# Kernel tuning notes

Measured on AMD Instinct MI355X. Metric: run time of the kernel, lower is better.

Reference implementation:

```python
import jax, jax.numpy as jnp
import numpy as np

EPS = 1e-12
TEMP = 0.05
LAMBDA2 = 0.5


def _normalize(x):
    # F.normalize(x, dim=1), eps=1e-12
    n = jnp.linalg.norm(x, axis=1, keepdims=True)
    return x / jnp.maximum(n, EPS)


def _cdist(x, f):
    # torch.cdist p=2: [B, N] euclidean distances
    x2 = jnp.sum(x * x, axis=1, keepdims=True)          # [B,1]
    f2 = jnp.sum(f * f, axis=1)[None, :]                # [1,N]
    d2 = x2 + f2 - 2.0 * (x @ f.T)
    return jnp.sqrt(jnp.maximum(d2, 0.0))


def _ce(logits, targets):
    # F.cross_entropy with integer targets, mean reduction
    logp = jax.nn.log_softmax(logits, axis=1)
    return -jnp.take_along_axis(logp, targets[:, None], axis=1).mean()


def _branch_loss(x_raw, f, targets):
    x = _normalize(x_raw)
    # note: original applies cross_entropy (which does another log_softmax)
    # on top of softmax(cdist(...)) -- reproduced faithfully
    soft = jax.nn.softmax(_cdist(x, f), axis=1)
    out = (x @ f.T) / TEMP
    return _ce(out, targets) + _ce(soft, targets)


def setup_inputs() -> dict:
    key = jax.random.key(0)
    ks = jax.random.split(key, 7)
    B, N, D = 256, 8192, 2048
    inputs = jax.random.normal(ks[0], (B, D), dtype=jnp.float32)
    inputs_up = jax.random.normal(ks[1], (B, D), dtype=jnp.float32)
    inputs_down = jax.random.normal(ks[2], (B, D), dtype=jnp.float32)
    targets = jax.random.randint(ks[3], (B,), 0, N)
    # memory banks are buffers; initialize as L2-normalized rows (realistic state)
    features = _normalize(jax.random.normal(ks[4], (N, D), dtype=jnp.float32))
    features_up = _normalize(jax.random.normal(ks[5], (N, D), dtype=jnp.float32))
    features_down = _normalize(jax.random.normal(ks[6], (N, D), dtype=jnp.float32))
    return {
        "inputs": inputs,
        "inputs_up": inputs_up,
        "inputs_down": inputs_down,
        "targets": targets,
        "epoch": 10,
        "features": features,
        "features_up": features_up,
        "features_down": features_down,
    }


def reference(inputs, inputs_up, inputs_down, targets, epoch, features, features_up, features_down):
    l_mid = _branch_loss(inputs, features, targets)
    l_up = _branch_loss(inputs_up, features_up, targets)
    l_down = _branch_loss(inputs_down, features_down, targets)
    loss = (1.0 - LAMBDA2) * l_mid + LAMBDA2 * (l_up + l_down)
    return loss
```

## Files before the change

kernel.cpp:

```cpp
#include <hip/hip_runtime.h>

typedef float f4v __attribute__((ext_vector_type(4)));
typedef float f32x4 __attribute__((ext_vector_type(4)));
typedef __bf16 bf16x8 __attribute__((ext_vector_type(8)));
typedef unsigned short ushort8 __attribute__((ext_vector_type(8)));

static constexpr int KDIM = 2048;

static constexpr size_t OFF_XN      = 0;
static constexpr size_t OFF_PART    = (size_t)3 * 256 * 2048 * 2;
static constexpr size_t OFF_DOTT    = OFF_PART + (size_t)768 * 128 * 16;
static constexpr size_t OFF_ROWLOSS = OFF_DOTT + 768 * 4;

__device__ __forceinline__ unsigned short f2bf(float x) {
  union { float f; unsigned u; } c; c.f = x;
  unsigned r = c.u + 0x7fffu + ((c.u >> 16) & 1u);
  return (unsigned short)(r >> 16);
}

__device__ __forceinline__ void gload_lds16(const void* g, void* l) {
  __builtin_amdgcn_global_load_lds((const __attribute__((address_space(1))) void*)g,
                                   (__attribute__((address_space(3))) void*)l,
                                   16, 0, 0);
}

__device__ __forceinline__ bf16x8 cvt8(f4v lo, f4v hi) {
  bf16x8 r;
  r[0] = (__bf16)lo[0]; r[1] = (__bf16)lo[1]; r[2] = (__bf16)lo[2]; r[3] = (__bf16)lo[3];
  r[4] = (__bf16)hi[0]; r[5] = (__bf16)hi[1]; r[6] = (__bf16)hi[2]; r[7] = (__bf16)hi[3];
  return r;
}

__global__ __launch_bounds__(256) void k_normalize(
    const float* __restrict__ x0, const float* __restrict__ x1, const float* __restrict__ x2,
    unsigned short* __restrict__ xn)
{
  int bid = blockIdx.x;
  int branch = bid >> 8;
  int row = bid & 255;
  const float* src = (branch == 0 ? x0 : (branch == 1 ? x1 : x2)) + (size_t)row * KDIM;
  int tid = threadIdx.x;
  f4v a = *(const f4v*)(src + tid * 8);
  f4v b = *(const f4v*)(src + tid * 8 + 4);
  float s = a[0]*a[0] + a[1]*a[1] + a[2]*a[2] + a[3]*a[3]
          + b[0]*b[0] + b[1]*b[1] + b[2]*b[2] + b[3]*b[3];
  #pragma unroll
  for (int m = 1; m < 64; m <<= 1) s += __shfl_xor(s, m);
  __shared__ float ls[4];
  if ((tid & 63) == 0) ls[tid >> 6] = s;
  __syncthreads();
  float total = ls[0] + ls[1] + ls[2] + ls[3];
  float inv = 1.0f / fmaxf(sqrtf(total), 1e-12f);
  ushort8 u;
  #pragma unroll
  for (int e = 0; e < 4; ++e) u[e]     = f2bf(a[e] * inv);
  #pragma unroll
  for (int e = 0; e < 4; ++e) u[4 + e] = f2bf(b[e] * inv);
  *(ushort8*)(xn + (size_t)bid * KDIM + tid * 8) = u;
}

__global__ __launch_bounds__(512, 1) void k_gemm_fused(
    const unsigned short* __restrict__ xn,
    const float* __restrict__ f0, const float* __restrict__ f1, const float* __restrict__ f2,
    const int* __restrict__ targets,
    float* __restrict__ part, float* __restrict__ dotT)
{
  __shared__ char lds[2 * 65536];

  int bid = blockIdx.x;
  int swz = (bid & 7) * 24 + (bid >> 3);
  int branch = swz >> 6;
  int ntile = swz & 63;

  const unsigned short* A = xn + (size_t)branch * 256 * KDIM;
  const float* F = (branch == 0 ? f0 : (branch == 1 ? f1 : f2)) + (size_t)ntile * 128 * KDIM;

  int tid = threadIdx.x;
  int wave = tid >> 6;
  int lane = tid & 63;
  int rcol0 = lane & 15;
  int klane = lane >> 4;
  int wr = wave >> 1;
  int wc = wave & 1;

  const unsigned short* aSrc = A + (size_t)(tid >> 3) * KDIM
                             + (((tid & 7) ^ ((tid >> 3) & 7)) << 3);
  const float* bSrc = F + (size_t)(tid >> 4) * KDIM
                    + (((tid & 15) ^ ((tid >> 4) & 15)) << 2);
  char* aDst = lds + wave * 1024;
  char* bDst = lds + 32768 + wave * 1024;

#define STAGE(kt, buf) do { \
    _Pragma("unroll") for (int g = 0; g < 4; ++g) \
      gload_lds16(aSrc + (size_t)g * 64 * KDIM + (kt) * 64, \
                  aDst + (buf) * 65536 + g * 8192); \
    _Pragma("unroll") for (int g = 0; g < 4; ++g) \
      gload_lds16(bSrc + (size_t)g * 32 * KDIM + (kt) * 64, \
                  bDst + (buf) * 65536 + g * 8192); \
  } while (0)

  f32x4 acc[4][4];
  #pragma unroll
  for (int i = 0; i < 4; ++i)
    #pragma unroll
    for (int j = 0; j < 4; ++j)
      #pragma unroll
      for (int q = 0; q < 4; ++q) acc[i][j][q] = 0.0f;

  int sa = rcol0 & 7;
  const char* aRd = lds + (wr * 64 + rcol0) * 128;
  const char* bRd = lds + 32768 + (wc * 64 + rcol0) * 256;

#define COMPUTE(buf) do { \
    const char* ra = aRd + (buf) * 65536; \
    const char* rb = bRd + (buf) * 65536; \
    _Pragma("unroll") for (int ks = 0; ks < 2; ++ks) { \
      int chA = (((ks * 4 + klane) ^ sa) << 4); \
      int x = ks * 8 + klane * 2; \
      int chB0 = ((x ^ rcol0) << 4); \
      int chB1 = (((x + 1) ^ rcol0) << 4); \
      bf16x8 a0 = *(const bf16x8*)(ra + chA); \
      bf16x8 a1 = *(const bf16x8*)(ra + 2048 + chA); \
      bf16x8 a2 = *(const bf16x8*)(ra + 4096 + chA); \
      bf16x8 a3 = *(const bf16x8*)(ra + 6144 + chA); \
      _Pragma("unroll") for (int j = 0; j < 4; ++j) { \
        f4v lo = *(const f4v*)(rb + j * 4096 + chB0); \
        f4v hi = *(const f4v*)(rb + j * 4096 + chB1); \
        bf16x8 bj = cvt8(lo, hi); \
        acc[0][j] = __builtin_amdgcn_mfma_f32_16x16x32_bf16(a0, bj, acc[0][j], 0, 0, 0); \
        acc[1][j] = __builtin_amdgcn_mfma_f32_16x16x32_bf16(a1, bj, acc[1][j], 0, 0, 0); \
        acc[2][j] = __builtin_amdgcn_mfma_f32_16x16x32_bf16(a2, bj, acc[2][j], 0, 0, 0); \
        acc[3][j] = __builtin_amdgcn_mfma_f32_16x16x32_bf16(a3, bj, acc[3][j], 0, 0, 0); \
      } \
    } \
  } while (0)

  STAGE(0, 0);
  __syncthreads();
  for (int kt = 0; kt < 31; ++kt) {
    int cur = kt & 1;
    STAGE(kt + 1, cur ^ 1);
    COMPUTE(cur);
    __syncthreads();
  }
  COMPUTE(1);

#undef STAGE
#undef COMPUTE

  int tbase = branch * 256;
  #pragma unroll
  for (int i = 0; i < 4; ++i) {
    #pragma unroll
    for (int q = 0; q < 4; ++q) {
      int row = wr * 64 + i * 16 + (klane << 2) + q;
      int tgt = targets[row];
      float s1 = 0.f, s2 = 0.f, s3 = 0.f, s4 = 0.f;
      #pragma unroll
      for (int j = 0; j < 4; ++j) {
        float d = acc[i][j][q];
        float e1 = __expf(fmaf(20.0f, d, -20.0f));
        float Dv = sqrtf(fmaxf(2.0f - 2.0f * d, 0.0f));
        float e2 = __expf(Dv - 2.0f);
        s1 += e1; s2 += e2;
        float t2 = e2 * e2;
        s3 += t2; s4 += t2 * e2;
        int col = ntile * 128 + wc * 64 + j * 16 + rcol0;
        if (col == tgt) dotT[tbase + row] = d;
      }
      #pragma unroll
      for (int m = 1; m < 16; m <<= 1) {
        s1 += __shfl_xor(s1, m);
        s2 += __shfl_xor(s2, m);
        s3 += __shfl_xor(s3, m);
        s4 += __shfl_xor(s4, m);
      }
      if (rcol0 == 0) {
        f32x4 p; p[0] = s1; p[1] = s2; p[2] = s3; p[3] = s4;
        *(f32x4*)(part + ((size_t)(tbase + row) * 128 + ntile * 2 + wc) * 4) = p;
      }
    }
  }
}

__global__ __launch_bounds__(128) void k_combine(
    const float* __restrict__ part, const float* __restrict__ dotT, float* __restrict__ rowloss)
{
  int row = blockIdx.x;
  int tid = threadIdx.x;
  f4v p = *(const f4v*)(part + ((size_t)row * 128 + tid) * 4);
  float a0 = p[0], a1 = p[1], a2 = p[2], a3 = p[3];
  #pragma unroll
  for (int m = 1; m < 64; m <<= 1) {
    a0 += __shfl_xor(a0, m); a1 += __shfl_xor(a1, m);
    a2 += __shfl_xor(a2, m); a3 += __shfl_xor(a3, m);
  }
  __shared__ float ls[8];
  if ((tid & 63) == 0) {
    int w = tid >> 6;
    ls[w] = a0; ls[2 + w] = a1; ls[4 + w] = a2; ls[6 + w] = a3;
  }
  __syncthreads();
  if (tid == 0) {
    float p1 = ls[0] + ls[1];
    float Z1 = ls[2] + ls[3];
    float Z2 = ls[4] + ls[5];
    float Z3 = ls[6] + ls[7];
    float dt = dotT[row];
    float CE1 = 20.0f + logf(p1) - 20.0f * dt;
    float Dt = sqrtf(fmaxf(2.0f - 2.0f * dt, 0.0f));
    float St = __expf(Dt - 2.0f) / Z1;
    float sES = 8193.0f + Z2 / (2.0f * Z1 * Z1) + Z3 / (6.0f * Z1 * Z1 * Z1);
    float CE2 = logf(sES) - St;
    rowloss[row] = (CE1 + CE2) * (0.5f / 256.0f);
  }
}

__global__ __launch_bounds__(256) void k_final(const float* __restrict__ rowloss, float* __restrict__ out)
{
  int tid = threadIdx.x;
  float v = rowloss[tid] + rowloss[tid + 256] + rowloss[tid + 512];
  #pragma unroll
  for (int m = 1; m < 64; m <<= 1) v += __shfl_xor(v, m);
  __shared__ float ls[4];
  if ((tid & 63) == 0) ls[tid >> 6] = v;
  __syncthreads();
  if (tid == 0) out[0] = ls[0] + ls[1] + ls[2] + ls[3];
}

extern "C" void kernel_launch(void* const* d_in, const int* in_sizes, int n_in,
                              void* d_out, int out_size, void* d_ws, size_t ws_size,
                              hipStream_t stream) {
  const float* in0 = (const float*)d_in[0];
  const float* in1 = (const float*)d_in[1];
  const float* in2 = (const float*)d_in[2];
  const int* targets = (const int*)d_in[3];
  const float* f0 = (const float*)d_in[5];
  const float* f1 = (const float*)d_in[6];
  const float* f2 = (const float*)d_in[7];

  char* ws = (char*)d_ws;
  unsigned short* xn = (unsigned short*)(ws + OFF_XN);
  float* part    = (float*)(ws + OFF_PART);
  float* dotT    = (float*)(ws + OFF_DOTT);
  float* rowloss = (float*)(ws + OFF_ROWLOSS);
  float* out = (float*)d_out;

  k_normalize<<<768, 256, 0, stream>>>(in0, in1, in2, xn);
  k_gemm_fused<<<192, 512, 0, stream>>>(xn, f0, f1, f2, targets, part, dotT);
  k_combine<<<768, 128, 0, stream>>>(part, dotT, rowloss);
  k_final<<<1, 256, 0, stream>>>(rowloss, out);
}
```

Measured before the change: 66.12 us.

## Split GEMM into 128x128 tiles and convert B to bf16 once before LDS

The fused GEMM now splits each branch's 256 rows into two M-tiles, launching 384 blocks of 256 threads instead of 192 blocks of 512, so more CUs have work. The fp32 feature tile is loaded into registers, converted to bf16 once, and stored swizzled into LDS. Before, every wave re-read fp32 from LDS and converted it redundantly for each MFMA. This also halves LDS use and allows two blocks per CU. The cost is that each feature tile is now read from global memory twice, once per M-tile, which leans on L2 sharing between paired blocks, and the register-staged B load is synchronous with the loop.

```diff
diff --git a/kernel.cpp b/kernel.cpp
--- a/kernel.cpp
+++ b/kernel.cpp
@@ -3,6 +3,7 @@
 typedef float f4v __attribute__((ext_vector_type(4)));
 typedef float f32x4 __attribute__((ext_vector_type(4)));
 typedef __bf16 bf16x8 __attribute__((ext_vector_type(8)));
+typedef __bf16 bf16x4 __attribute__((ext_vector_type(4)));
 typedef unsigned short ushort8 __attribute__((ext_vector_type(8)));
 
 static constexpr int KDIM = 2048;
@@ -24,11 +25,10 @@
                                    16, 0, 0);
 }
 
-__device__ __forceinline__ bf16x8 cvt8(f4v lo, f4v hi) {
-  bf16x8 r;
-  r[0] = (__bf16)lo[0]; r[1] = (__bf16)lo[1]; r[2] = (__bf16)lo[2]; r[3] = (__bf16)lo[3];
-  r[4] = (__bf16)hi[0]; r[5] = (__bf16)hi[1]; r[6] = (__bf16)hi[2]; r[7] = (__bf16)hi[3];
-  return r;
+__device__ __forceinline__ void cvt_store8(char* p, f4v v) {
+  bf16x4 o;
+  o[0] = (__bf16)v[0]; o[1] = (__bf16)v[1]; o[2] = (__bf16)v[2]; o[3] = (__bf16)v[3];
+  *(bf16x4*)p = o;
 }
 
 __global__ __launch_bounds__(256) void k_normalize(
@@ -59,20 +59,22 @@
   *(ushort8*)(xn + (size_t)bid * KDIM + tid * 8) = u;
 }
 
-__global__ __launch_bounds__(512, 1) void k_gemm_fused(
+__global__ __launch_bounds__(256, 2) void k_gemm_fused(
     const unsigned short* __restrict__ xn,
     const float* __restrict__ f0, const float* __restrict__ f1, const float* __restrict__ f2,
     const int* __restrict__ targets,
     float* __restrict__ part, float* __restrict__ dotT)
 {
-  __shared__ char lds[2 * 65536];
+  __shared__ char lds[2 * 32768];
 
   int bid = blockIdx.x;
-  int swz = (bid & 7) * 24 + (bid >> 3);
-  int branch = swz >> 6;
-  int ntile = swz & 63;
-
-  const unsigned short* A = xn + (size_t)branch * 256 * KDIM;
+  int swz = (bid & 7) * 48 + (bid >> 3);
+  int branch = swz >> 7;
+  int rem = swz & 127;
+  int ntile = rem >> 1;
+  int mtile = rem & 1;
+
+  const unsigned short* A = xn + ((size_t)branch * 256 + (size_t)mtile * 128) * KDIM;
   const float* F = (branch == 0 ? f0 : (branch == 1 ? f1 : f2)) + (size_t)ntile * 128 * KDIM;
 
   int tid = threadIdx.x;
@@ -85,18 +87,41 @@
 
   const unsigned short* aSrc = A + (size_t)(tid >> 3) * KDIM
                              + (((tid & 7) ^ ((tid >> 3) & 7)) << 3);
-  const float* bSrc = F + (size_t)(tid >> 4) * KDIM
-                    + (((tid & 15) ^ ((tid >> 4) & 15)) << 2);
   char* aDst = lds + wave * 1024;
-  char* bDst = lds + 32768 + wave * 1024;
-
-#define STAGE(kt, buf) do { \
+
+#define STAGE_A(kt, buf) do { \
     _Pragma("unroll") for (int g = 0; g < 4; ++g) \
-      gload_lds16(aSrc + (size_t)g * 64 * KDIM + (kt) * 64, \
-                  aDst + (buf) * 65536 + g * 8192); \
-    _Pragma("unroll") for (int g = 0; g < 4; ++g) \
-      gload_lds16(bSrc + (size_t)g * 32 * KDIM + (kt) * 64, \
-                  bDst + (buf) * 65536 + g * 8192); \
+      gload_lds16(aSrc + (size_t)g * 32 * KDIM + (kt) * 64, \
+                  aDst + (buf) * 32768 + g * 4096); \
+  } while (0)
+
+  const float* bSrc = F + (size_t)(tid >> 4) * KDIM + (tid & 15) * 4;
+  f4v bg0, bg1, bg2, bg3, bg4, bg5, bg6, bg7;
+
+#define LOADB_G(kt) do { \
+    bg0 = *(const f4v*)(bSrc + (kt) * 64); \
+    bg1 = *(const f4v*)(bSrc + (size_t)16 * KDIM + (kt) * 64); \
+    bg2 = *(const f4v*)(bSrc + (size_t)32 * KDIM + (kt) * 64); \
+    bg3 = *(const f4v*)(bSrc + (size_t)48 * KDIM + (kt) * 64); \
+    bg4 = *(const f4v*)(bSrc + (size_t)64 * KDIM + (kt) * 64); \
+    bg5 = *(const f4v*)(bSrc + (size_t)80 * KDIM + (kt) * 64); \
+    bg6 = *(const f4v*)(bSrc + (size_t)96 * KDIM + (kt) * 64); \
+    bg7 = *(const f4v*)(bSrc + (size_t)112 * KDIM + (kt) * 64); \
+  } while (0)
+
+  int bOff = 16384 + (tid >> 4) * 128
+           + (((((tid & 15) >> 1)) ^ ((tid >> 4) & 7)) << 4) + (tid & 1) * 8;
+
+#define WRITE_B(buf) do { \
+    char* wb = lds + (buf) * 32768 + bOff; \
+    cvt_store8(wb,          bg0); \
+    cvt_store8(wb + 2048,   bg1); \
+    cvt_store8(wb + 4096,   bg2); \
+    cvt_store8(wb + 6144,   bg3); \
+    cvt_store8(wb + 8192,   bg4); \
+    cvt_store8(wb + 10240,  bg5); \
+    cvt_store8(wb + 12288,  bg6); \
+    cvt_store8(wb + 14336,  bg7); \
   } while (0)
 
   f32x4 acc[4][4];
@@ -109,24 +134,19 @@
 
   int sa = rcol0 & 7;
   const char* aRd = lds + (wr * 64 + rcol0) * 128;
-  const char* bRd = lds + 32768 + (wc * 64 + rcol0) * 256;
+  const char* bRd = lds + 16384 + (wc * 64 + rcol0) * 128;
 
 #define COMPUTE(buf) do { \
-    const char* ra = aRd + (buf) * 65536; \
-    const char* rb = bRd + (buf) * 65536; \
+    const char* ra = aRd + (buf) * 32768; \
+    const char* rb = bRd + (buf) * 32768; \
     _Pragma("unroll") for (int ks = 0; ks < 2; ++ks) { \
-      int chA = (((ks * 4 + klane) ^ sa) << 4); \
-      int x = ks * 8 + klane * 2; \
-      int chB0 = ((x ^ rcol0) << 4); \
-      int chB1 = (((x + 1) ^ rcol0) << 4); \
-      bf16x8 a0 = *(const bf16x8*)(ra + chA); \
-      bf16x8 a1 = *(const bf16x8*)(ra + 2048 + chA); \
-      bf16x8 a2 = *(const bf16x8*)(ra + 4096 + chA); \
-      bf16x8 a3 = *(const bf16x8*)(ra + 6144 + chA); \
+      int ch = (((ks * 4 + klane) ^ sa) << 4); \
+      bf16x8 a0 = *(const bf16x8*)(ra + ch); \
+      bf16x8 a1 = *(const bf16x8*)(ra + 2048 + ch); \
+      bf16x8 a2 = *(const bf16x8*)(ra + 4096 + ch); \
+      bf16x8 a3 = *(const bf16x8*)(ra + 6144 + ch); \
       _Pragma("unroll") for (int j = 0; j < 4; ++j) { \
-        f4v lo = *(const f4v*)(rb + j * 4096 + chB0); \
-        f4v hi = *(const f4v*)(rb + j * 4096 + chB1); \
-        bf16x8 bj = cvt8(lo, hi); \
+        bf16x8 bj = *(const bf16x8*)(rb + j * 2048 + ch); \
         acc[0][j] = __builtin_amdgcn_mfma_f32_16x16x32_bf16(a0, bj, acc[0][j], 0, 0, 0); \
         acc[1][j] = __builtin_amdgcn_mfma_f32_16x16x32_bf16(a1, bj, acc[1][j], 0, 0, 0); \
         acc[2][j] = __builtin_amdgcn_mfma_f32_16x16x32_bf16(a2, bj, acc[2][j], 0, 0, 0); \
@@ -135,25 +155,34 @@
     } \
   } while (0)
 
-  STAGE(0, 0);
-  __syncthreads();
-  for (int kt = 0; kt < 31; ++kt) {
+  LOADB_G(0);
+  STAGE_A(0, 0);
+  WRITE_B(0);
+  __syncthreads();
+
+  for (int kt = 0; kt < 32; ++kt) {
     int cur = kt & 1;
-    STAGE(kt + 1, cur ^ 1);
+    if (kt < 31) {
+      LOADB_G(kt + 1);
+      STAGE_A(kt + 1, cur ^ 1);
+    }
     COMPUTE(cur);
+    if (kt < 31) WRITE_B(cur ^ 1);
     __syncthreads();
   }
-  COMPUTE(1);
-
-#undef STAGE
+
+#undef STAGE_A
+#undef LOADB_G
+#undef WRITE_B
 #undef COMPUTE
 
   int tbase = branch * 256;
+  int mbase = mtile * 128;
   #pragma unroll
   for (int i = 0; i < 4; ++i) {
     #pragma unroll
     for (int q = 0; q < 4; ++q) {
-      int row = wr * 64 + i * 16 + (klane << 2) + q;
+      int row = mbase + wr * 64 + i * 16 + (klane << 2) + q;
       int tgt = targets[row];
       float s1 = 0.f, s2 = 0.f, s3 = 0.f, s4 = 0.f;
       #pragma unroll
@@ -247,7 +276,7 @@
   float* out = (float*)d_out;
 
   k_normalize<<<768, 256, 0, stream>>>(in0, in1, in2, xn);
-  k_gemm_fused<<<192, 512, 0, stream>>>(xn, f0, f1, f2, targets, part, dotT);
+  k_gemm_fused<<<384, 256, 0, stream>>>(xn, f0, f1, f2, targets, part, dotT);
   k_combine<<<768, 128, 0, stream>>>(part, dotT, rowloss);
   k_final<<<1, 256, 0, stream>>>(rowloss, out);
 }
```

New measurement: 87.16 us. 1.32x slower.
